# Performance work log

Measured on AMD Instinct MI355X. Metric: run time of the kernel, lower is better.

The kernel has to match this reference:

```python
import jax, jax.numpy as jnp
import numpy as np

KERNEL_SIZES = (3, 5, 7)
NUM_HEAD = 6
DIM = 192
K_SCALES = 3
HEADS_PER_SCALE = NUM_HEAD // K_SCALES  # 2
HEAD_DIM = DIM // NUM_HEAD              # 32
SCALE = HEAD_DIM ** -0.5


def _nbr_idx(L, K):
    # NATTEN non-causal, dilation=1: window centered on query, clamped at edges.
    start = jnp.clip(jnp.arange(L) - K // 2, 0, L - K)
    return start[:, None] + jnp.arange(K)  # [L, K]


def _na3d_branch(xi, K):
    # xi: [B, D, H, W, C] with C = 3 * HEADS_PER_SCALE * HEAD_DIM
    B, D, H, W, C = xi.shape
    qkv = xi.reshape(B, D, H, W, 3, HEADS_PER_SCALE, HEAD_DIM).transpose(4, 0, 5, 1, 2, 3, 6)
    q, k, v = qkv[0] * SCALE, qkv[1], qkv[2]  # each [B, h, D, H, W, hd]

    idd, idh, idw = _nbr_idx(D, K), _nbr_idx(H, K), _nbr_idx(W, K)

    def gather(t):
        t = jnp.take(t, idd, axis=2)  # [B,h,D,K,H,W,hd]
        t = jnp.take(t, idh, axis=4)  # [B,h,D,K,H,K,W,hd]
        t = jnp.take(t, idw, axis=6)  # [B,h,D,K,H,K,W,K,hd]
        return t

    kn = gather(k)
    vn = gather(v)
    # attention logits over the K^3 neighborhood per query
    attn = jnp.einsum('bndhwc,bndihjwkc->bndhwijk', q, kn)
    attn = jax.nn.softmax(attn.reshape(B, HEADS_PER_SCALE, D, H, W, K ** 3), axis=-1)
    attn = attn.reshape(B, HEADS_PER_SCALE, D, H, W, K, K, K)
    y = jnp.einsum('bndhwijk,bndihjwkc->bndhwc', attn, vn)
    # [B,h,D,H,W,hd] -> [B,D,H,W,h*hd]
    return y.transpose(0, 2, 3, 4, 1, 5).reshape(B, D, H, W, HEADS_PER_SCALE * HEAD_DIM)


def setup_inputs() -> dict:
    key = jax.random.key(0)
    k0, k1, k2 = jax.random.split(key, 3)
    x = jax.random.normal(k0, (1, 8, 24, 24, DIM), dtype=jnp.float32)
    W_qkv = jax.random.normal(k1, (DIM, 3 * DIM), dtype=jnp.float32) * 0.02
    b_qkv = jnp.zeros((3 * DIM,), dtype=jnp.float32)
    W_proj = jax.random.normal(k2, (DIM, DIM), dtype=jnp.float32) * 0.02
    b_proj = jnp.zeros((DIM,), dtype=jnp.float32)
    return {'x': x, 'W_qkv': W_qkv, 'b_qkv': b_qkv, 'W_proj': W_proj, 'b_proj': b_proj}


def reference(x, W_qkv, b_qkv, W_proj, b_proj):
    qkv = x @ W_qkv + b_qkv  # [B,D,H,W,3*DIM]
    # torch.split with channels [DIM, DIM, DIM]
    chunks = jnp.split(qkv, K_SCALES, axis=4)
    ys = [_na3d_branch(chunks[i], KERNEL_SIZES[i]) for i in range(K_SCALES)]
    y = jnp.concatenate(ys, axis=4)  # [B,D,H,W,DIM]
    return y @ W_proj + b_proj
```

## Files before the change

kernel.cpp:

```cpp
#include <hip/hip_runtime.h>

typedef unsigned short ushort_t;
typedef unsigned int uint_t;
typedef __attribute__((ext_vector_type(8))) short short8;
typedef __attribute__((ext_vector_type(4))) float f32x4;

constexpr int DD = 8, HH = 24, WW = 24;
constexpr int NQ = DD * HH * WW;
constexpr int CIN = 192;
constexpr int CQKV = 576;
constexpr int KP = 576;
constexpr float ATT_SCALE = 0.17677669529663687f;
constexpr int NROW = DD * HH;

__device__ __forceinline__ ushort_t bf16h(float x) {
    uint_t u = __float_as_uint(x);
    u += 0x7FFFu + ((u >> 16) & 1u);
    return (ushort_t)(u >> 16);
}
__device__ __forceinline__ float bf16f(ushort_t h) {
    return __uint_as_float(((uint_t)h) << 16);
}
__device__ __forceinline__ float2 unpack2(uint_t u) {
    return make_float2(__uint_as_float(u << 16),
                       __uint_as_float(u & 0xffff0000u));
}

constexpr int EB0 = 0;
constexpr int EB1 = NROW * 2 * WW * 2;
constexpr int EB2 = EB1 + NROW * 3 * WW * 2;
constexpr int ETOT = EB2 + NROW * 4 * WW * 2;

__global__ __launch_bounds__(256)
void convert_w_kernel(const float* __restrict__ Wq, const float* __restrict__ Wp,
                      ushort_t* __restrict__ Bq, ushort_t* __restrict__ Bp)
{
    __shared__ float T[32][36];
    int b = blockIdx.x;
    const float* W; ushort_t* Bb; int N;
    int kt, nt;
    if (b < 108) { W = Wq; Bb = Bq; N = CQKV; kt = b % 6; nt = b / 6; }
    else         { b -= 108; W = Wp; Bb = Bp; N = CIN; kt = b % 6; nt = b / 6; }
    const int k0 = kt * 32, n0 = nt * 32;
    const int tid = threadIdx.x;

    #pragma unroll
    for (int p = 0; p < 4; ++p) {
        int e = p * 256 + tid;
        int r = e >> 5, c = e & 31;
        T[c][r] = W[(long)(k0 + r) * N + n0 + c];
    }
    __syncthreads();
    const int n = tid >> 3;
    const int k4 = (tid & 7) * 4;
    float4 v = *(const float4*)(&T[n][k4]);
    ushort4 hv, lv;
    hv.x = bf16h(v.x); lv.x = bf16h(v.x - bf16f(hv.x));
    hv.y = bf16h(v.y); lv.y = bf16h(v.y - bf16f(hv.y));
    hv.z = bf16h(v.z); lv.z = bf16h(v.z - bf16f(hv.z));
    hv.w = bf16h(v.w); lv.w = bf16h(v.w - bf16f(hv.w));
    const int k = k0 + k4;
    const int g = k >> 6;
    const int kc = k & 63;
    ushort_t* row = Bb + (long)(n0 + n) * KP + g * 192 + kc;
    *(ushort4*)(row)       = hv;
    *(ushort4*)(row + 64)  = lv;
    *(ushort4*)(row + 128) = hv;
}

template<bool BF16OUT>
__global__ __launch_bounds__(256)
void gemm_mfma_kernel(const float* __restrict__ A, const ushort_t* __restrict__ Bb,
                      const float* __restrict__ bias, void* __restrict__ Cout, int N)
{
    __shared__ ushort_t As[64][72];
    __shared__ ushort_t Bs[64][72];
    __shared__ float Ct[64][68];

    const int tid = threadIdx.x;
    const int bm = blockIdx.x * 64;
    const int bn = blockIdx.y * 64;

    const int wv = tid >> 6;
    const int lane = tid & 63;
    const int lm = lane & 15;
    const int quad = lane >> 4;
    const int wr = (wv >> 1) * 32;
    const int wc = (wv & 1) * 32;

    const int ar = tid >> 4;
    const int ac4 = (tid & 15) * 4;
    const int br0 = tid >> 3;
    const int bc0 = (tid & 7) * 8;

    f32x4 acc[2][2] = {};

    #pragma unroll
    for (int g = 0; g < 3; ++g) {
        float4 av[4];
        ushort4 hv4[4];
        #pragma unroll
        for (int p = 0; p < 4; ++p)
            av[p] = *(const float4*)(A + (long)(bm + ar + p * 16) * CIN + g * 64 + ac4);

        #pragma unroll
        for (int ph = 0; ph < 3; ++ph) {
            const int kk = g * 192 + ph * 64;
            uint4 b0 = *(const uint4*)(Bb + (long)(bn + br0) * KP + kk + bc0);
            uint4 b1 = *(const uint4*)(Bb + (long)(bn + br0 + 32) * KP + kk + bc0);
            __syncthreads();
            if (ph == 0) {
                #pragma unroll
                for (int p = 0; p < 4; ++p) {
                    float4 v = av[p];
                    ushort4 hv;
                    hv.x = bf16h(v.x); hv.y = bf16h(v.y);
                    hv.z = bf16h(v.z); hv.w = bf16h(v.w);
                    hv4[p] = hv;
                    *(ushort4*)(&As[ar + p * 16][ac4]) = hv;
                }
            } else if (ph == 2) {
                #pragma unroll
                for (int p = 0; p < 4; ++p) {
                    float4 v = av[p];
                    ushort4 lv;
                    lv.x = bf16h(v.x - bf16f(hv4[p].x));
                    lv.y = bf16h(v.y - bf16f(hv4[p].y));
                    lv.z = bf16h(v.z - bf16f(hv4[p].z));
                    lv.w = bf16h(v.w - bf16f(hv4[p].w));
                    *(ushort4*)(&As[ar + p * 16][ac4]) = lv;
                }
            }
            *(uint4*)(&Bs[br0][bc0]) = b0;
            *(uint4*)(&Bs[br0 + 32][bc0]) = b1;
            __syncthreads();

            #pragma unroll
            for (int ks = 0; ks < 64; ks += 32) {
                short8 af0 = *(const short8*)(&As[wr + lm][ks + quad * 8]);
                short8 af1 = *(const short8*)(&As[wr + 16 + lm][ks + quad * 8]);
                short8 bf0 = *(const short8*)(&Bs[wc + lm][ks + quad * 8]);
                short8 bf1 = *(const short8*)(&Bs[wc + 16 + lm][ks + quad * 8]);
                acc[0][0] = __builtin_amdgcn_mfma_f32_16x16x32_bf16(af0, bf0, acc[0][0], 0, 0, 0);
                acc[0][1] = __builtin_amdgcn_mfma_f32_16x16x32_bf16(af0, bf1, acc[0][1], 0, 0, 0);
                acc[1][0] = __builtin_amdgcn_mfma_f32_16x16x32_bf16(af1, bf0, acc[1][0], 0, 0, 0);
                acc[1][1] = __builtin_amdgcn_mfma_f32_16x16x32_bf16(af1, bf1, acc[1][1], 0, 0, 0);
            }
        }
    }

    #pragma unroll
    for (int tc = 0; tc < 2; ++tc) {
        const float bv = bias[bn + wc + tc * 16 + lm];
        #pragma unroll
        for (int tr = 0; tr < 2; ++tr) {
            #pragma unroll
            for (int reg = 0; reg < 4; ++reg)
                Ct[wr + tr * 16 + quad * 4 + reg][wc + tc * 16 + lm] = acc[tr][tc][reg] + bv;
        }
    }
    __syncthreads();
    const int orow = tid >> 4;
    const int oc4 = (tid & 15) * 4;
    #pragma unroll
    for (int p = 0; p < 4; ++p) {
        const int r = orow + p * 16;
        float4 v = *(const float4*)(&Ct[r][oc4]);
        if (BF16OUT) {
            ushort4 hv;
            hv.x = bf16h(v.x); hv.y = bf16h(v.y); hv.z = bf16h(v.z); hv.w = bf16h(v.w);
            *(ushort4*)((ushort_t*)Cout + (long)(bm + r) * N + bn + oc4) = hv;
        } else {
            *(float4*)((float*)Cout + (long)(bm + r) * N + bn + oc4) = v;
        }
    }
}

constexpr int KROW = 72;
constexpr int RBUF = WW * KROW;

template<int K>
__device__ __forceinline__
void split_chunk(const ushort_t* __restrict__ qkv,
                 float* __restrict__ accs, float* __restrict__ stats,
                 int r, int c, int nchunks, int scale, int ebase,
                 int w, int hd, int d8, int tid,
                 ushort_t* __restrict__ ksh, ushort_t* __restrict__ vsh)
{
    const int i0 = 2 * c;
    const int ni = (K - i0) < 2 ? (K - i0) : 2;
    const int NT = ni * K;

    const int dq = r / HH, hq = r % HH;
    int sd = dq - K / 2; sd = sd < 0 ? 0 : (sd > DD - K ? DD - K : sd);
    int sh = hq - K / 2; sh = sh < 0 ? 0 : (sh > HH - K ? HH - K : sh);
    int sw = w  - K / 2; sw = sw < 0 ? 0 : (sw > WW - K ? WW - K : sw);

    const int q = (dq * HH + hq) * WW + w;

    uint4 qu = *(const uint4*)(qkv + (long)q * CQKV + scale * 192 + hd * 32 + d8 * 8);
    float2 qf[4] = {unpack2(qu.x), unpack2(qu.y), unpack2(qu.z), unpack2(qu.w)};
    #pragma unroll
    for (int t = 0; t < 4; ++t) {
        qf[t].x *= ATT_SCALE;
        qf[t].y *= ATT_SCALE;
    }

    const int lw = tid >> 3;
    const int c8 = (tid & 7) * 8;

    auto load_kv = [&](int buf, int t) {
        int i = i0 + t / K;
        int j = t - (t / K) * K;
        const ushort_t* p = qkv + (long)(((sd + i) * HH + (sh + j)) * WW + lw) * CQKV
                          + scale * 192 + c8;
        uint4 kk = *(const uint4*)(p + 64);
        uint4 vv = *(const uint4*)(p + 128);
        *(uint4*)(ksh + buf * RBUF + lw * KROW + c8) = kk;
        *(uint4*)(vsh + buf * RBUF + lw * KROW + c8) = vv;
    };

    float sum = 0.f;
    float2 acc[4] = {};
    const int choff = hd * 32 + d8 * 8;

    load_kv(0, 0);
    if (NT > 1) load_kv(1, 1);

    for (int t = 0; t < NT; ++t) {
        __syncthreads();
        if (t + 2 < NT) load_kv((t + 2) % 3, t + 2);

        const ushort_t* kb = ksh + (t % 3) * RBUF + choff;
        const ushort_t* vb = vsh + (t % 3) * RBUF + choff;
        #pragma unroll
        for (int n = 0; n < K; ++n) {
            uint4 ku = *(const uint4*)(kb + (sw + n) * KROW);
            float2 k0 = unpack2(ku.x), k1 = unpack2(ku.y),
                   k2 = unpack2(ku.z), k3 = unpack2(ku.w);
            float2 d;
            d.x  = qf[0].x * k0.x; d.y  = qf[0].y * k0.y;
            d.x += qf[1].x * k1.x; d.y += qf[1].y * k1.y;
            d.x += qf[2].x * k2.x; d.y += qf[2].y * k2.y;
            d.x += qf[3].x * k3.x; d.y += qf[3].y * k3.y;
            float p = d.x + d.y;
            p += __shfl_xor(p, 1);
            p += __shfl_xor(p, 2);
            float pr = __expf(p);
            sum += pr;
            uint4 vu = *(const uint4*)(vb + (sw + n) * KROW);
            float2 v0 = unpack2(vu.x), v1 = unpack2(vu.y),
                   v2 = unpack2(vu.z), v3 = unpack2(vu.w);
            acc[0].x += pr * v0.x; acc[0].y += pr * v0.y;
            acc[1].x += pr * v1.x; acc[1].y += pr * v1.y;
            acc[2].x += pr * v2.x; acc[2].y += pr * v2.y;
            acc[3].x += pr * v3.x; acc[3].y += pr * v3.y;
        }
    }

    const int e = ebase + ((r * nchunks + c) * WW + w) * 2 + hd;
    if (d8 == 0) {
        stats[2 * e]     = 0.0f;
        stats[2 * e + 1] = sum;
    }
    float* ap = accs + (long)e * 32 + d8 * 8;
    *(float4*)(ap)     = make_float4(acc[0].x, acc[0].y, acc[1].x, acc[1].y);
    *(float4*)(ap + 4) = make_float4(acc[2].x, acc[2].y, acc[3].x, acc[3].y);
}

__global__ __launch_bounds__(192)
void na3d_split_kernel(const ushort_t* __restrict__ qkv,
                       float* __restrict__ accs, float* __restrict__ stats)
{
    __shared__ alignas(16) ushort_t ksh[3 * RBUF];
    __shared__ alignas(16) ushort_t vsh[3 * RBUF];

    const int tid = threadIdx.x;
    const int w  = tid >> 3;
    const int hd = (tid >> 2) & 1;
    const int d8 = tid & 3;

    const int bid = blockIdx.x;
    if (bid < NROW * 4) {
        int r = bid >> 2, c = bid & 3;
        split_chunk<7>(qkv, accs, stats, r, c, 4, 2, EB2, w, hd, d8, tid, ksh, vsh);
    } else if (bid < NROW * 4 + NROW * 3) {
        int t = bid - NROW * 4;
        int r = t / 3, c = t - (t / 3) * 3;
        split_chunk<5>(qkv, accs, stats, r, c, 3, 1, EB1, w, hd, d8, tid, ksh, vsh);
    } else {
        int t = bid - NROW * 7;
        int r = t >> 1, c = t & 1;
        split_chunk<3>(qkv, accs, stats, r, c, 2, 0, EB0, w, hd, d8, tid, ksh, vsh);
    }
}

__global__ __launch_bounds__(256)
void na3d_combine_kernel(const float* __restrict__ accs,
                         const float* __restrict__ stats,
                         float* __restrict__ y)
{
    const int n = blockIdx.x * 256 + threadIdx.x;
    constexpr int PER_SCALE = NROW * WW * 2 * 8;
    const int scale = n / PER_SCALE;
    const int rem = n - scale * PER_SCALE;
    const int d4 = rem & 7;
    const int hd = (rem >> 3) & 1;
    const int t  = rem >> 4;
    const int w  = t % WW;
    const int row = t / WW;

    const int CK = scale == 0 ? 2 : (scale == 1 ? 3 : 4);
    const int ebase = scale == 0 ? EB0 : (scale == 1 ? EB1 : EB2);

    float mv[4], sv[4];
    float M = -1e30f;
    for (int c = 0; c < CK; ++c) {
        int e = ebase + ((row * CK + c) * WW + w) * 2 + hd;
        mv[c] = stats[2 * e];
        sv[c] = stats[2 * e + 1];
        M = fmaxf(M, mv[c]);
    }
    float S = 0.f;
    float4 o = make_float4(0.f, 0.f, 0.f, 0.f);
    for (int c = 0; c < CK; ++c) {
        int e = ebase + ((row * CK + c) * WW + w) * 2 + hd;
        float wgt = __expf(mv[c] - M);
        S += sv[c] * wgt;
        float4 a = *(const float4*)(accs + (long)e * 32 + d4 * 4);
        o.x += wgt * a.x; o.y += wgt * a.y; o.z += wgt * a.z; o.w += wgt * a.w;
    }
    const float rs = 1.0f / S;
    o.x *= rs; o.y *= rs; o.z *= rs; o.w *= rs;

    const int q = row * WW + w;
    *(float4*)(y + (long)q * CIN + scale * 64 + hd * 32 + d4 * 4) = o;
}

extern "C" void kernel_launch(void* const* d_in, const int* in_sizes, int n_in,
                              void* d_out, int out_size, void* d_ws, size_t ws_size,
                              hipStream_t stream)
{
    const float* x      = (const float*)d_in[0];
    const float* W_qkv  = (const float*)d_in[1];
    const float* b_qkv  = (const float*)d_in[2];
    const float* W_proj = (const float*)d_in[3];
    const float* b_proj = (const float*)d_in[4];
    float* out = (float*)d_out;

    float* accs    = (float*)d_ws;
    float* stats   = accs + (long)ETOT * 32;
    float* y       = stats + 2 * ETOT;
    ushort_t* qkvb = (ushort_t*)(y + (long)NQ * CIN);
    ushort_t* Wbq  = qkvb + (long)NQ * CQKV;
    ushort_t* Wbp  = Wbq + (long)CQKV * KP;

    convert_w_kernel<<<dim3(144), 256, 0, stream>>>(W_qkv, W_proj, Wbq, Wbp);

    gemm_mfma_kernel<true><<<dim3(NQ / 64, CQKV / 64), 256, 0, stream>>>(x, Wbq, b_qkv, qkvb, CQKV);

    na3d_split_kernel<<<dim3(NROW * (4 + 3 + 2)), 192, 0, stream>>>(qkvb, accs, stats);

    na3d_combine_kernel<<<dim3(3 * NQ * 16 / 256), 256, 0, stream>>>(accs, stats, y);

    gemm_mfma_kernel<false><<<dim3(NQ / 64, CIN / 64), 256, 0, stream>>>(y, Wbp, b_proj, out, CIN);
}
```

Baseline: 115.7 us.

## Fuse split-softmax combine into projection GEMM and remap split-kernel block order

Removes the separate combine kernel and the fp32 y buffer by having the output projection GEMM read the partial accumulators and softmax sums directly. It normalises them in registers and splits them into hi/lo bf16 A tiles for the MFMA. Stats now store only the sum, because max is always zero, which removes the max/exp rescaling. The split kernel's block index is also permuted with a stride-8 interleave, likely to spread neighbouring rows across XCDs for cache locality. The cost is that the combine work is recomputed in each of the three column-block tiles of the projection.

```diff
diff --git a/kernel.cpp b/kernel.cpp
--- a/kernel.cpp
+++ b/kernel.cpp
@@ -68,10 +68,9 @@
     *(ushort4*)(row + 128) = hv;
 }
 
-template<bool BF16OUT>
 __global__ __launch_bounds__(256)
 void gemm_mfma_kernel(const float* __restrict__ A, const ushort_t* __restrict__ Bb,
-                      const float* __restrict__ bias, void* __restrict__ Cout, int N)
+                      const float* __restrict__ bias, ushort_t* __restrict__ Cout, int N)
 {
     __shared__ ushort_t As[64][72];
     __shared__ ushort_t Bs[64][72];
@@ -166,13 +165,133 @@
     for (int p = 0; p < 4; ++p) {
         const int r = orow + p * 16;
         float4 v = *(const float4*)(&Ct[r][oc4]);
-        if (BF16OUT) {
-            ushort4 hv;
-            hv.x = bf16h(v.x); hv.y = bf16h(v.y); hv.z = bf16h(v.z); hv.w = bf16h(v.w);
-            *(ushort4*)((ushort_t*)Cout + (long)(bm + r) * N + bn + oc4) = hv;
-        } else {
-            *(float4*)((float*)Cout + (long)(bm + r) * N + bn + oc4) = v;
-        }
+        ushort4 hv;
+        hv.x = bf16h(v.x); hv.y = bf16h(v.y); hv.z = bf16h(v.z); hv.w = bf16h(v.w);
+        *(ushort4*)(Cout + (long)(bm + r) * N + bn + oc4) = hv;
+    }
+}
+
+__global__ __launch_bounds__(256)
+void gemm_proj_kernel(const float* __restrict__ accs, const float* __restrict__ stats,
+                      const ushort_t* __restrict__ Bb, const float* __restrict__ bias,
+                      float* __restrict__ Cout)
+{
+    __shared__ ushort_t As[64][72];
+    __shared__ ushort_t Bs[64][72];
+    __shared__ float Ct[64][68];
+
+    const int tid = threadIdx.x;
+    const int bm = blockIdx.x * 64;
+    const int bn = blockIdx.y * 64;
+
+    const int wv = tid >> 6;
+    const int lane = tid & 63;
+    const int lm = lane & 15;
+    const int quad = lane >> 4;
+    const int wr = (wv >> 1) * 32;
+    const int wc = (wv & 1) * 32;
+
+    const int ar = tid >> 4;
+    const int ac4 = (tid & 15) * 4;
+    const int a_hd = ac4 >> 5;
+    const int a_cc = ac4 & 31;
+    const int br0 = tid >> 3;
+    const int bc0 = (tid & 7) * 8;
+
+    f32x4 acc[2][2] = {};
+
+    #pragma unroll
+    for (int g = 0; g < 3; ++g) {
+        const int CK = g + 2;
+        const int eb = (g == 0) ? EB0 : (g == 1 ? EB1 : EB2);
+
+        float4 av[4];
+        ushort4 hv4[4];
+        #pragma unroll
+        for (int p = 0; p < 4; ++p) {
+            const int q = bm + ar + p * 16;
+            const int rr = q / WW;
+            const int w = q - rr * WW;
+            const int e0 = eb + (rr * CK) * (WW * 2) + w * 2 + a_hd;
+            float S = 0.f;
+            float4 a = make_float4(0.f, 0.f, 0.f, 0.f);
+            #pragma unroll
+            for (int c = 0; c < 4; ++c) {
+                if (c < CK) {
+                    const int e = e0 + c * (WW * 2);
+                    S += stats[e];
+                    const float4 t = *(const float4*)(accs + (long)e * 32 + a_cc);
+                    a.x += t.x; a.y += t.y; a.z += t.z; a.w += t.w;
+                }
+            }
+            const float rs = 1.0f / S;
+            av[p] = make_float4(a.x * rs, a.y * rs, a.z * rs, a.w * rs);
+        }
+
+        #pragma unroll
+        for (int ph = 0; ph < 3; ++ph) {
+            const int kk = g * 192 + ph * 64;
+            uint4 b0 = *(const uint4*)(Bb + (long)(bn + br0) * KP + kk + bc0);
+            uint4 b1 = *(const uint4*)(Bb + (long)(bn + br0 + 32) * KP + kk + bc0);
+            __syncthreads();
+            if (ph == 0) {
+                #pragma unroll
+                for (int p = 0; p < 4; ++p) {
+                    float4 v = av[p];
+                    ushort4 hv;
+                    hv.x = bf16h(v.x); hv.y = bf16h(v.y);
+                    hv.z = bf16h(v.z); hv.w = bf16h(v.w);
+                    hv4[p] = hv;
+                    *(ushort4*)(&As[ar + p * 16][ac4]) = hv;
+                }
+            } else if (ph == 2) {
+                #pragma unroll
+                for (int p = 0; p < 4; ++p) {
+                    float4 v = av[p];
+                    ushort4 lv;
+                    lv.x = bf16h(v.x - bf16f(hv4[p].x));
+                    lv.y = bf16h(v.y - bf16f(hv4[p].y));
+                    lv.z = bf16h(v.z - bf16f(hv4[p].z));
+                    lv.w = bf16h(v.w - bf16f(hv4[p].w));
+                    *(ushort4*)(&As[ar + p * 16][ac4]) = lv;
+                }
+            }
+            *(uint4*)(&Bs[br0][bc0]) = b0;
+            *(uint4*)(&Bs[br0 + 32][bc0]) = b1;
+            __syncthreads();
+
+            #pragma unroll
+            for (int ks = 0; ks < 64; ks += 32) {
+                short8 af0 = *(const short8*)(&As[wr + lm][ks + quad * 8]);
+                short8 af1 = *(const short8*)(&As[wr + 16 + lm][ks + quad * 8]);
+                short8 bf0 = *(const short8*)(&Bs[wc + lm][ks + quad * 8]);
+                short8 bf1 = *(const short8*)(&Bs[wc + 16 + lm][ks + quad * 8]);
+                acc[0][0] = __builtin_amdgcn_mfma_f32_16x16x32_bf16(af0, bf0, acc[0][0], 0, 0, 0);
+                acc[0][1] = __builtin_amdgcn_mfma_f32_16x16x32_bf16(af0, bf1, acc[0][1], 0, 0, 0);
+                acc[1][0] = __builtin_amdgcn_mfma_f32_16x16x32_bf16(af1, bf0, acc[1][0], 0, 0, 0);
+                acc[1][1] = __builtin_amdgcn_mfma_f32_16x16x32_bf16(af1, bf1, acc[1][1], 0, 0, 0);
+            }
+        }
+    }
+
+    #pragma unroll
+    for (int tc = 0; tc < 2; ++tc) {
+        const float bv = bias[bn + wc + tc * 16 + lm];
+        #pragma unroll
+        for (int tr = 0; tr < 2; ++tr) {
+            #pragma unroll
+            for (int reg = 0; reg < 4; ++reg)
+                Ct[wr + tr * 16 + quad * 4 + reg][wc + tc * 16 + lm] = acc[tr][tc][reg] + bv;
+        }
+    }
+    __syncthreads();
+    const int orow = tid >> 4;
+    const int oc4 = (tid & 15) * 4;
+    #pragma unroll
+    for (int p = 0; p < 4; ++p) {
+        const int r = orow + p * 16;
+        float4 v = *(const float4*)(&Ct[r][oc4]);
+        *(float4*)(Cout + (long)(bm + r) * CIN + bn + oc4) = v;
     }
 }
 
@@ -259,10 +378,7 @@
     }
 
     const int e = ebase + ((r * nchunks + c) * WW + w) * 2 + hd;
-    if (d8 == 0) {
-        stats[2 * e]     = 0.0f;
-        stats[2 * e + 1] = sum;
-    }
+    if (d8 == 0) stats[e] = sum;
     float* ap = accs + (long)e * 32 + d8 * 8;
     *(float4*)(ap)     = make_float4(acc[0].x, acc[0].y, acc[1].x, acc[1].y);
     *(float4*)(ap + 4) = make_float4(acc[2].x, acc[2].y, acc[3].x, acc[3].y);
@@ -280,7 +396,18 @@
     const int hd = (tid >> 2) & 1;
     const int d8 = tid & 3;
 
-    const int bid = blockIdx.x;
+    const int orig = blockIdx.x;
+    int bid;
+    if (orig < NROW * 4) {
+        bid = (orig & 7) * (NROW * 4 / 8) + (orig >> 3);
+    } else if (orig < NROW * 7) {
+        const int t = orig - NROW * 4;
+        bid = NROW * 4 + (t & 7) * (NROW * 3 / 8) + (t >> 3);
+    } else {
+        const int t = orig - NROW * 7;
+        bid = NROW * 7 + (t & 7) * (NROW * 2 / 8) + (t >> 3);
+    }
+
     if (bid < NROW * 4) {
         int r = bid >> 2, c = bid & 3;
         split_chunk<7>(qkv, accs, stats, r, c, 4, 2, EB2, w, hd, d8, tid, ksh, vsh);
@@ -295,48 +422,6 @@
     }
 }
 
-__global__ __launch_bounds__(256)
-void na3d_combine_kernel(const float* __restrict__ accs,
-                         const float* __restrict__ stats,
-                         float* __restrict__ y)
-{
-    const int n = blockIdx.x * 256 + threadIdx.x;
-    constexpr int PER_SCALE = NROW * WW * 2 * 8;
-    const int scale = n / PER_SCALE;
-    const int rem = n - scale * PER_SCALE;
-    const int d4 = rem & 7;
-    const int hd = (rem >> 3) & 1;
-    const int t  = rem >> 4;
-    const int w  = t % WW;
-    const int row = t / WW;
-
-    const int CK = scale == 0 ? 2 : (scale == 1 ? 3 : 4);
-    const int ebase = scale == 0 ? EB0 : (scale == 1 ? EB1 : EB2);
-
-    float mv[4], sv[4];
-    float M = -1e30f;
-    for (int c = 0; c < CK; ++c) {
-        int e = ebase + ((row * CK + c) * WW + w) * 2 + hd;
-        mv[c] = stats[2 * e];
-        sv[c] = stats[2 * e + 1];
-        M = fmaxf(M, mv[c]);
-    }
-    float S = 0.f;
-    float4 o = make_float4(0.f, 0.f, 0.f, 0.f);
-    for (int c = 0; c < CK; ++c) {
-        int e = ebase + ((row * CK + c) * WW + w) * 2 + hd;
-        float wgt = __expf(mv[c] - M);
-        S += sv[c] * wgt;
-        float4 a = *(const float4*)(accs + (long)e * 32 + d4 * 4);
-        o.x += wgt * a.x; o.y += wgt * a.y; o.z += wgt * a.z; o.w += wgt * a.w;
-    }
-    const float rs = 1.0f / S;
-    o.x *= rs; o.y *= rs; o.z *= rs; o.w *= rs;
-
-    const int q = row * WW + w;
-    *(float4*)(y + (long)q * CIN + scale * 64 + hd * 32 + d4 * 4) = o;
-}
-
 extern "C" void kernel_launch(void* const* d_in, const int* in_sizes, int n_in,
                               void* d_out, int out_size, void* d_ws, size_t ws_size,
                               hipStream_t stream)
@@ -350,18 +435,15 @@
 
     float* accs    = (float*)d_ws;
     float* stats   = accs + (long)ETOT * 32;
-    float* y       = stats + 2 * ETOT;
-    ushort_t* qkvb = (ushort_t*)(y + (long)NQ * CIN);
+    ushort_t* qkvb = (ushort_t*)(stats + ETOT);
     ushort_t* Wbq  = qkvb + (long)NQ * CQKV;
     ushort_t* Wbp  = Wbq + (long)CQKV * KP;
 
     convert_w_kernel<<<dim3(144), 256, 0, stream>>>(W_qkv, W_proj, Wbq, Wbp);
 
-    gemm_mfma_kernel<true><<<dim3(NQ / 64, CQKV / 64), 256, 0, stream>>>(x, Wbq, b_qkv, qkvb, CQKV);
+    gemm_mfma_kernel<<<dim3(NQ / 64, CQKV / 64), 256, 0, stream>>>(x, Wbq, b_qkv, qkvb, CQKV);
 
     na3d_split_kernel<<<dim3(NROW * (4 + 3 + 2)), 192, 0, stream>>>(qkvb, accs, stats);
 
-    na3d_combine_kernel<<<dim3(3 * NQ * 16 / 256), 256, 0, stream>>>(accs, stats, y);
-
-    gemm_mfma_kernel<false><<<dim3(NQ / 64, CIN / 64), 256, 0, stream>>>(y, Wbp, b_proj, out, CIN);
-}
+    gemm_proj_kernel<<<dim3(NQ / 64, CIN / 64), 256, 0, stream>>>(accs, stats, Wbp, b_proj, out);
+}
```

After: 111.7 us. 3.5% less time.
